# Optimization experiments

Measured on AMD Instinct MI355X. Metric: run time of the kernel, lower is better.

The kernel has to match this reference:

```python
import jax, jax.numpy as jnp
import numpy as np

C = 64  # channels fixed by module

def conv1x1(x, W, b):
    # x: [B,C,H,W], W: [C_out,C_in], b: [C_out]
    return jnp.einsum('bchw,oc->bohw', x, W) + b[None, :, None, None]

def setup_inputs() -> dict:
    key = jax.random.key(0)
    ks = jax.random.split(key, 16)
    B, H, W = 4, 64, 64
    inp = {
        'x_latter': jax.random.normal(ks[0], (B, C, H, W), jnp.float32),
        'x': jax.random.normal(ks[1], (B, C, H, W), jnp.float32),
    }
    scale = 1.0 / np.sqrt(C)
    names = ['high', 'low', 'value', 'e_conv', 'mid', 'latter']
    for i, n in enumerate(names):
        inp[f'W_{n}'] = jax.random.normal(ks[2 + 2 * i], (C, C), jnp.float32) * scale
        inp[f'b_{n}'] = jax.random.normal(ks[3 + 2 * i], (C,), jnp.float32) * 0.01
    return inp

def reference(x_latter, x, W_high, b_high, W_low, b_low, W_value, b_value,
              W_e_conv, b_e_conv, W_mid, b_mid, W_latter, b_latter):
    b, c, h, w = x_latter.shape
    hw = h * w
    # stage 1: channel-normalized spatial attention
    xl_hi = conv1x1(x_latter, W_high, b_high).reshape(b, c, hw)          # [b,c,hw]
    x_low = conv1x1(x, W_low, b_low).reshape(b, c, hw).transpose(0, 2, 1)  # [b,hw,c]
    p = jnp.einsum('bnc,bcm->bnm', x_low, xl_hi)                          # [b,hw,hw]
    p = jax.nn.softmax(p, axis=1)  # torch Softmax(dim=1) over first hw axis
    v = conv1x1(x, W_value, b_value).reshape(b, c, hw).transpose(0, 2, 1)  # [b,hw,c]
    e = jnp.einsum('bnm,bmc->bnc', p, v) + x_low                          # [b,hw,c]
    e = e.transpose(0, 2, 1).reshape(b, c, h, w)                          # [b,c,h,w]
    e = conv1x1(e, W_e_conv, b_e_conv).reshape(b, c, hw)                  # [b,c,hw]
    # stage 2: channel-channel attention
    xl2 = conv1x1(x_latter, W_latter, b_latter).reshape(b, c, hw).transpose(0, 2, 1)  # [b,hw,c]
    t = jnp.einsum('bcn,bnd->bcd', e, xl2)                                # [b,c,c]
    t = jax.nn.softmax(t, axis=1)
    x_mid = conv1x1(x, W_mid, b_mid).reshape(b, c, hw).transpose(0, 2, 1)  # [b,hw,c]
    out = jnp.einsum('bnc,bcd->bnd', x_mid, t)                            # [b,hw,c]
    return out.transpose(0, 2, 1).reshape(b, c, h, w)
```

## Files before the change

### kernel.cpp

```cpp
#include <hip/hip_runtime.h>
#include <math.h>

#define BATCH 4
#define CH 64
#define HW 4096
#define LOG2E 1.4426950408889634f

typedef __attribute__((ext_vector_type(8))) short short8;
typedef __attribute__((ext_vector_type(4))) float f32x4;
typedef __attribute__((ext_vector_type(4))) float float4v;
typedef __attribute__((ext_vector_type(4))) unsigned int uint4v;

#define MFMA(a, b, c) __builtin_amdgcn_mfma_f32_16x16x32_bf16(a, b, c, 0, 0, 0)

__device__ __forceinline__ float exp2v(float x) {
#if __has_builtin(__builtin_amdgcn_exp2f)
    return __builtin_amdgcn_exp2f(x);
#else
    return exp2f(x);
#endif
}
__device__ __forceinline__ void cvtpk2(float a, float b, unsigned &h, unsigned &l) {
    unsigned hv;
    asm("v_cvt_pk_bf16_f32 %0, %1, %2" : "=v"(hv) : "v"(a), "v"(b));
    float ra = a - __builtin_bit_cast(float, hv << 16);
    float rb = b - __builtin_bit_cast(float, hv & 0xffff0000u);
    unsigned lv;
    asm("v_cvt_pk_bf16_f32 %0, %1, %2" : "=v"(lv) : "v"(ra), "v"(rb));
    h = hv; l = lv;
}
__device__ __forceinline__ void gld16(const short* g, short* l) {
    __builtin_amdgcn_global_load_lds(
        (const __attribute__((address_space(1))) unsigned int*)g,
        (__attribute__((address_space(3))) unsigned int*)l, 16, 0, 0);
}

__global__ __launch_bounds__(256) void convm(
    const float* __restrict__ x, const float* __restrict__ xl,
    const float* __restrict__ Wlow, const float* __restrict__ blow,
    const float* __restrict__ Wval, const float* __restrict__ bval,
    const float* __restrict__ Wmid, const float* __restrict__ bmid,
    const float* __restrict__ Wlat, const float* __restrict__ blat,
    const float* __restrict__ Whigh, const float* __restrict__ bhigh,
    float* __restrict__ XLOW, float* __restrict__ XMID, float* __restrict__ XL2,
    short* __restrict__ PAh, short* __restrict__ PAl,
    short* __restrict__ PBh, short* __restrict__ PBl,
    short* __restrict__ PVh, short* __restrict__ PVl)
{
    int mode = blockIdx.z, b = blockIdx.y, bx = blockIdx.x;
    const float* W; const float* bias; const float* X;
    switch (mode) {
        case 0:  W = Wlow;  bias = blow;  X = x;  break;
        case 1:  W = Wval;  bias = bval;  X = x;  break;
        case 2:  W = Wmid;  bias = bmid;  X = x;  break;
        case 3:  W = Wlat;  bias = blat;  X = xl; break;
        default: W = Whigh; bias = bhigh; X = xl; break;
    }
    int t = threadIdx.x, wv = t >> 6, ln = t & 63;
    int row = ln & 15, g = ln >> 4;

    short8 Wh[4][2], Wlo[4][2];
    #pragma unroll
    for (int ot = 0; ot < 4; ot++)
        #pragma unroll
        for (int kt = 0; kt < 2; kt++) {
            const float* wp = W + (ot * 16 + row) * 64 + kt * 32 + g * 8;
            uint4v hw, lw;
            #pragma unroll
            for (int k2 = 0; k2 < 4; k2++) {
                unsigned h, l;
                cvtpk2(wp[2 * k2], wp[2 * k2 + 1], h, l);
                hw[k2] = h; lw[k2] = l;
            }
            Wh[ot][kt] = __builtin_bit_cast(short8, hw);
            Wlo[ot][kt] = __builtin_bit_cast(short8, lw);
        }

    int nt = bx * 4 + wv;
    short8 Bh[2], Bl[2];
    #pragma unroll
    for (int kt = 0; kt < 2; kt++) {
        float v[8];
        #pragma unroll
        for (int j = 0; j < 8; j++)
            v[j] = X[(size_t)(b * 64 + kt * 32 + g * 8 + j) * HW + nt * 16 + row];
        uint4v hw, lw;
        #pragma unroll
        for (int k2 = 0; k2 < 4; k2++) {
            unsigned h, l;
            cvtpk2(v[2 * k2], v[2 * k2 + 1], h, l);
            hw[k2] = h; lw[k2] = l;
        }
        Bh[kt] = __builtin_bit_cast(short8, hw);
        Bl[kt] = __builtin_bit_cast(short8, lw);
    }

    f32x4 acc[4];
    #pragma unroll
    for (int ot = 0; ot < 4; ot++) {
        #pragma unroll
        for (int r = 0; r < 4; r++) acc[ot][r] = bias[ot * 16 + g * 4 + r];
    }
    #pragma unroll
    for (int ot = 0; ot < 4; ot++)
        #pragma unroll
        for (int kt = 0; kt < 2; kt++) {
            acc[ot] = MFMA(Wh[ot][kt], Bh[kt], acc[ot]);
            acc[ot] = MFMA(Wh[ot][kt], Bl[kt], acc[ot]);
            acc[ot] = MFMA(Wlo[ot][kt], Bh[kt], acc[ot]);
        }

    __shared__ float Ld[64][65];
    #pragma unroll
    for (int ot = 0; ot < 4; ot++)
        #pragma unroll
        for (int r = 0; r < 4; r++)
            Ld[wv * 16 + (ln & 15)][ot * 16 + g * 4 + r] = acc[ot][r];
    __syncthreads();

    int n0 = bx * 64;
    if (mode == 0 || mode == 2 || mode == 3) {
        float* outp = (mode == 0) ? XLOW : (mode == 2) ? XMID : XL2;
        int n = t >> 2, o0 = (t & 3) * 16;
        float vout[16];
        #pragma unroll
        for (int k = 0; k < 16; k++) vout[k] = Ld[n][o0 + k];
        float* gp = outp + ((size_t)b * HW + n0 + n) * 64 + o0;
        #pragma unroll
        for (int k = 0; k < 4; k++)
            *(float4v*)(gp + k * 4) = *(float4v*)(vout + k * 4);
    }
    if (mode == 0 || mode == 4) {
        short* Ph = (mode == 0) ? PAh : PBh;
        short* Pl = (mode == 0) ? PAl : PBl;
        float scale = (mode == 4) ? LOG2E : 1.0f;
        #pragma unroll
        for (int kt = 0; kt < 2; kt++) {
            uint4v hw, lw;
            #pragma unroll
            for (int k2 = 0; k2 < 4; k2++) {
                unsigned h, l;
                cvtpk2(Ld[wv * 16 + (ln & 15)][kt * 32 + g * 8 + 2 * k2] * scale,
                       Ld[wv * 16 + (ln & 15)][kt * 32 + g * 8 + 2 * k2 + 1] * scale, h, l);
                hw[k2] = h; lw[k2] = l;
            }
            size_t blob = (((size_t)b * 256 + bx * 4 + wv) * 2 + kt) * 512 + (size_t)ln * 8;
            *(uint4v*)(Ph + blob) = hw;
            *(uint4v*)(Pl + blob) = lw;
        }
    }
    if (mode == 1) {
        int ktm_l = wv >> 1;
        int ct0 = (wv & 1) * 2;
        #pragma unroll
        for (int cc = 0; cc < 2; cc++) {
            int ct = ct0 + cc;
            int c = ct * 16 + (ln & 15);
            float v[8];
            #pragma unroll
            for (int j = 0; j < 8; j++)
                v[j] = Ld[(ktm_l * 2 + (j >> 2)) * 16 + g * 4 + (j & 3)][c];
            uint4v hw, lw;
            #pragma unroll
            for (int k2 = 0; k2 < 4; k2++) {
                unsigned h, l;
                cvtpk2(v[2 * k2], v[2 * k2 + 1], h, l);
                hw[k2] = h; lw[k2] = l;
            }
            size_t blob = (((size_t)b * 128 + bx * 2 + ktm_l) * 4 + ct) * 512 + (size_t)ln * 8;
            *(uint4v*)(PVh + blob) = hw;
            *(uint4v*)(PVl + blob) = lw;
        }
    }
}

__global__ __launch_bounds__(256) void zpass2(
    const short* __restrict__ PAh, const short* __restrict__ PAl,
    const short* __restrict__ PBh, const short* __restrict__ PBl,
    float* __restrict__ Zp)
{
    int bid = blockIdx.x;
    int sw = (bid & 7) * 128 + (bid >> 3);
    int mchunk = sw & 63, nc = (sw >> 6) & 3, b = sw >> 8;
    int t = threadIdx.x, wv = t >> 6, ln = t & 63;
    short8 bh[4][2], bl[4][2];
    #pragma unroll
    for (int msub = 0; msub < 4; msub++)
        #pragma unroll
        for (int kt = 0; kt < 2; kt++) {
            size_t o = ((size_t)(b * 256 + mchunk * 4 + msub) * 2 + kt) * 512 + ln * 8;
            bh[msub][kt] = *(const short8*)(PBh + o);
            bl[msub][kt] = *(const short8*)(PBl + o);
        }
    float zacc[4] = {0.f, 0.f, 0.f, 0.f};
    for (int s = 0; s < 16; s++) {
        int nt = nc * 64 + s * 4 + wv;
        size_t ab = ((size_t)(b * 256 + nt) * 2) * 512 + ln * 8;
        short8 ah0 = *(const short8*)(PAh + ab);
        short8 ah1 = *(const short8*)(PAh + ab + 512);
        short8 al0 = *(const short8*)(PAl + ab);
        short8 al1 = *(const short8*)(PAl + ab + 512);
        #pragma unroll
        for (int msub = 0; msub < 4; msub++) {
            f32x4 acc = {0.f, 0.f, 0.f, 0.f};
            acc = MFMA(ah0, bh[msub][0], acc);
            acc = MFMA(ah1, bh[msub][1], acc);
            acc = MFMA(ah0, bl[msub][0], acc);
            acc = MFMA(ah1, bl[msub][1], acc);
            acc = MFMA(al0, bh[msub][0], acc);
            acc = MFMA(al1, bh[msub][1], acc);
            zacc[msub] += exp2v(acc[0]) + exp2v(acc[1]) + exp2v(acc[2]) + exp2v(acc[3]);
        }
    }
    #pragma unroll
    for (int msub = 0; msub < 4; msub++) {
        zacc[msub] += __shfl_xor(zacc[msub], 16, 64);
        zacc[msub] += __shfl_xor(zacc[msub], 32, 64);
    }
    __shared__ float sZ[4][64];
    if (ln < 16) {
        #pragma unroll
        for (int msub = 0; msub < 4; msub++) sZ[wv][msub * 16 + ln] = zacc[msub];
    }
    __syncthreads();
    if (t < 64) {
        float z = sZ[0][t] + sZ[1][t] + sZ[2][t] + sZ[3][t];
        Zp[((size_t)(b * 4 + nc)) * 4096 + mchunk * 64 + t] = z;
    }
}

__global__ __launch_bounds__(256, 3) void epass10(
    const short* __restrict__ PAh, const short* __restrict__ PAl,
    const short* __restrict__ PBh, const short* __restrict__ PBl,
    const short* __restrict__ PVh, const short* __restrict__ PVl,
    const float* __restrict__ Zp, float* __restrict__ Ep, int nseg)
{
    int nwg = 32 * nseg * 4, cpx = nwg >> 3;
    int bid = blockIdx.x;
    int sw = (bid & 7) * cpx + (bid >> 3);
    int nb = sw & 31, mseg = (sw >> 5) % nseg, b = sw / (32 * nseg);
    int iters = 128 / nseg;
    int mper = 4096 / nseg;
    int t = threadIdx.x, wv = t >> 6, ln = t & 63;
    int lnm = ln & 15, lnr = ln >> 4;

    __shared__ __align__(16) short sB[2][2][2048];
    __shared__ __align__(16) short sV[2][2][2048];
    __shared__ __align__(16) float sZi[1024];

    for (int k = t; k < mper; k += 256) {
        int m = mseg * mper + k;
        float z = Zp[((size_t)(b * 4 + 0)) * 4096 + m]
                + Zp[((size_t)(b * 4 + 1)) * 4096 + m]
                + Zp[((size_t)(b * 4 + 2)) * 4096 + m]
                + Zp[((size_t)(b * 4 + 3)) * 4096 + m];
        sZi[k] = 1.f / z;
    }

    short8 Lh[2][2], Ll[2][2];
    #pragma unroll
    for (int rt = 0; rt < 2; rt++)
        #pragma unroll
        for (int kt = 0; kt < 2; kt++) {
            int nt = nb * 8 + wv * 2 + rt;
            size_t base = ((size_t)(b * 256 + nt) * 2 + kt) * 512 + ln * 8;
            Lh[rt][kt] = *(const short8*)(PAh + base);
            Ll[rt][kt] = *(const short8*)(PAl + base);
        }

    f32x4 acc_e[2][4];
    #pragma unroll
    for (int rt = 0; rt < 2; rt++)
        #pragma unroll
        for (int ct = 0; ct < 4; ct++) acc_e[rt][ct] = (f32x4){0.f, 0.f, 0.f, 0.f};

    const int mt00 = mseg * (mper >> 4);
    const int ktm0 = mseg * (mper >> 5);
    #define STAGE(bufi, ii) { \
        size_t pbb = (size_t)b * 262144 + (size_t)(mt00 + (ii) * 2) * 1024; \
        size_t pvb = (size_t)b * 262144 + (size_t)(ktm0 + (ii)) * 2048; \
        gld16(PBh + pbb + t * 8, &sB[bufi][0][wv * 512]); \
        gld16(PBl + pbb + t * 8, &sB[bufi][1][wv * 512]); \
        gld16(PVh + pvb + t * 8, &sV[bufi][0][wv * 512]); \
        gld16(PVl + pvb + t * 8, &sV[bufi][1][wv * 512]); }

    STAGE(0, 0);
    __syncthreads();

    for (int i = 0; i < iters; i++) {
        int cur = i & 1;
        if (i + 1 < iters) STAGE(cur ^ 1, i + 1);

        f32x4 wf[2][2];
        #pragma unroll
        for (int ms = 0; ms < 2; ms++) {
            const short8 bh0 = *(const short8*)&sB[cur][0][(ms * 2 + 0) * 512 + ln * 8];
            const short8 bh1 = *(const short8*)&sB[cur][0][(ms * 2 + 1) * 512 + ln * 8];
            const short8 bl0 = *(const short8*)&sB[cur][1][(ms * 2 + 0) * 512 + ln * 8];
            const short8 bl1 = *(const short8*)&sB[cur][1][(ms * 2 + 1) * 512 + ln * 8];
            const f32x4 vz = *(const f32x4*)&sZi[i * 32 + ms * 16 + lnr * 4];
            __builtin_amdgcn_s_setprio(1);
            #pragma unroll
            for (int rt = 0; rt < 2; rt++) {
                f32x4 acc = {0.f, 0.f, 0.f, 0.f};
                acc = MFMA(bh0, Lh[rt][0], acc);
                acc = MFMA(bh1, Lh[rt][1], acc);
                acc = MFMA(bh0, Ll[rt][0], acc);
                acc = MFMA(bh1, Ll[rt][1], acc);
                acc = MFMA(bl0, Lh[rt][0], acc);
                acc = MFMA(bl1, Lh[rt][1], acc);
                #pragma unroll
                for (int r = 0; r < 4; r++)
                    wf[rt][ms][r] = exp2v(acc[r]) * vz[r];
            }
            __builtin_amdgcn_s_setprio(0);
        }
        short8 pah[2], pal[2];
        #pragma unroll
        for (int rt = 0; rt < 2; rt++) {
            uint4v hw, lw;
            #pragma unroll
            for (int k2 = 0; k2 < 4; k2++) {
                unsigned h, l;
                cvtpk2(wf[rt][k2 >> 1][2 * (k2 & 1)],
                       wf[rt][k2 >> 1][2 * (k2 & 1) + 1], h, l);
                hw[k2] = h; lw[k2] = l;
            }
            pah[rt] = __builtin_bit_cast(short8, hw);
            pal[rt] = __builtin_bit_cast(short8, lw);
        }
        __builtin_amdgcn_s_setprio(1);
        #pragma unroll
        for (int ct = 0; ct < 4; ct++) {
            const short8 vh = *(const short8*)&sV[cur][0][ct * 512 + ln * 8];
            const short8 vl = *(const short8*)&sV[cur][1][ct * 512 + ln * 8];
            #pragma unroll
            for (int rt = 0; rt < 2; rt++) {
                acc_e[rt][ct] = MFMA(pah[rt], vh, acc_e[rt][ct]);
                acc_e[rt][ct] = MFMA(pah[rt], vl, acc_e[rt][ct]);
                acc_e[rt][ct] = MFMA(pal[rt], vh, acc_e[rt][ct]);
            }
        }
        __builtin_amdgcn_s_setprio(0);
        __syncthreads();
    }
    #undef STAGE

    float* ep = Ep + ((size_t)mseg * BATCH + b) * HW * 64;
    #pragma unroll
    for (int rt = 0; rt < 2; rt++) {
        int n0 = (nb * 8 + wv * 2 + rt) * 16 + lnr * 4;
        #pragma unroll
        for (int ct = 0; ct < 4; ct++) {
            #pragma unroll
            for (int r = 0; r < 4; r++)
                ep[(size_t)(n0 + r) * 64 + ct * 16 + lnm] = acc_e[rt][ct][r];
        }
    }
}

template <int NSEG>
__global__ __launch_bounds__(256) void econv6(
    const float* __restrict__ Ep, const float* __restrict__ XLOW,
    const float* __restrict__ W, const float* __restrict__ bias,
    float* __restrict__ E2)
{
    const size_t SEG = (size_t)BATCH * HW * 64;
    int b = blockIdx.y, n0 = blockIdx.x * 64, t = threadIdx.x;
    __shared__ float Wl[64][64];
    __shared__ float El[64][65];
    for (int i = t; i < 4096; i += 256) Wl[i >> 6][i & 63] = W[i];
    for (int q = t; q < 1024; q += 256) {
        int nl = q >> 4, c0 = (q & 15) * 4;
        size_t idx = ((size_t)b * HW + n0 + nl) * 64 + c0;
        float4v s = *(const float4v*)(XLOW + idx);
        #pragma unroll
        for (int sg = 0; sg < NSEG; sg++) {
            float4v p = *(const float4v*)(Ep + sg * SEG + idx);
            s.x += p.x; s.y += p.y; s.z += p.z; s.w += p.w;
        }
        El[nl][c0] = s.x; El[nl][c0 + 1] = s.y;
        El[nl][c0 + 2] = s.z; El[nl][c0 + 3] = s.w;
    }
    __syncthreads();
    int nl = t & 63, og = t >> 6;
    for (int k = 0; k < 16; k++) {
        int o = og * 16 + k;
        float a0 = bias[o], a1 = 0.f, a2 = 0.f, a3 = 0.f;
        #pragma unroll
        for (int c = 0; c < 64; c += 4) {
            a0 += Wl[o][c]     * El[nl][c];
            a1 += Wl[o][c + 1] * El[nl][c + 1];
            a2 += Wl[o][c + 2] * El[nl][c + 2];
            a3 += Wl[o][c + 3] * El[nl][c + 3];
        }
        E2[((size_t)b * 64 + o) * HW + n0 + nl] = (a0 + a1) + (a2 + a3);
    }
}

__global__ __launch_bounds__(1024) void tmat(
    const float* __restrict__ E2, const float* __restrict__ XL2, float* __restrict__ T)
{
    int b = blockIdx.y, c = blockIdx.x, t = threadIdx.x;
    int d = t & 63, nl = t >> 6;
    const float* e = E2 + ((size_t)b * 64 + c) * HW;
    const float* x2 = XL2 + (size_t)b * HW * 64;
    float a0 = 0.f, a1 = 0.f;
    #pragma unroll 4
    for (int k = 0; k < 256; k += 2) {
        int na = k * 16 + nl, nb2 = na + 16;
        a0 += e[na] * x2[(size_t)na * 64 + d];
        a1 += e[nb2] * x2[(size_t)nb2 * 64 + d];
    }
    __shared__ float red[16][64];
    red[nl][d] = a0 + a1;
    __syncthreads();
    if (t < 64) {
        float s = 0.f;
        #pragma unroll
        for (int j = 0; j < 16; j++) s += red[j][t];
        T[((size_t)b * 64 + c) * 64 + t] = s;
    }
}

__global__ __launch_bounds__(64) void softT(
    const float* __restrict__ T, float* __restrict__ Ts)
{
    int d = blockIdx.x, b = blockIdx.y, c = threadIdx.x;
    float v = T[((size_t)b * 64 + c) * 64 + d];
    float M = v;
    #pragma unroll
    for (int o = 32; o > 0; o >>= 1) M = fmaxf(M, __shfl_xor(M, o, 64));
    float ez = __expf(v - M);
    float Z = ez;
    #pragma unroll
    for (int o = 32; o > 0; o >>= 1) Z += __shfl_xor(Z, o, 64);
    Ts[((size_t)b * 64 + c) * 64 + d] = ez / Z;
}

__global__ __launch_bounds__(256) void outk(
    const float* __restrict__ XMID, const float* __restrict__ Ts, float* __restrict__ out)
{
    int b = blockIdx.y, n0 = blockIdx.x * 64, t = threadIdx.x;
    __shared__ float Xm[64][65];
    __shared__ float Tl[64][64];
    for (int i = t; i < 4096; i += 256) {
        int nl = i >> 6, c = i & 63;
        Xm[nl][c] = XMID[((size_t)b * HW + n0 + nl) * 64 + c];
    }
    for (int i = t; i < 4096; i += 256) Tl[i >> 6][i & 63] = Ts[(size_t)b * 4096 + i];
    __syncthreads();
    int nl = t & 63, dg = t >> 6;
    float accs[16];
    #pragma unroll
    for (int k = 0; k < 16; k++) accs[k] = 0.f;
    for (int c = 0; c < 64; c++) {
        float xv = Xm[nl][c];
        #pragma unroll
        for (int k = 0; k < 16; k++) accs[k] += xv * Tl[c][dg * 16 + k];
    }
    #pragma unroll
    for (int k = 0; k < 16; k++) {
        int d = dg * 16 + k;
        out[((size_t)b * 64 + d) * HW + n0 + nl] = accs[k];
    }
}

extern "C" void kernel_launch(void* const* d_in, const int* in_sizes, int n_in,
                              void* d_out, int out_size, void* d_ws, size_t ws_size,
                              hipStream_t stream)
{
    const float* x_latter = (const float*)d_in[0];
    const float* x        = (const float*)d_in[1];
    const float* W_high = (const float*)d_in[2];  const float* b_high = (const float*)d_in[3];
    const float* W_low  = (const float*)d_in[4];  const float* b_low  = (const float*)d_in[5];
    const float* W_val  = (const float*)d_in[6];  const float* b_val  = (const float*)d_in[7];
    const float* W_ec   = (const float*)d_in[8];  const float* b_ec   = (const float*)d_in[9];
    const float* W_mid  = (const float*)d_in[10]; const float* b_mid  = (const float*)d_in[11];
    const float* W_lat  = (const float*)d_in[12]; const float* b_lat  = (const float*)d_in[13];
    float* outp = (float*)d_out;

    const size_t MAT = (size_t)BATCH * CH * HW;

    const size_t fixed_f = 3 * MAT + (size_t)BATCH * 4 * HW + 2 * (size_t)BATCH * 64 * 64;
    const size_t need8 = (fixed_f + 8 * MAT) * 4 + 6 * MAT * 2;
    int nseg = (ws_size >= need8) ? 8 : 4;

    float* ws = (float*)d_ws;
    size_t off = 0;
    float* XLOW = ws + off; off += MAT;
    float* XMID = ws + off; off += MAT;
    float* XL2  = ws + off; off += MAT;
    float* Zp   = ws + off; off += (size_t)BATCH * 4 * HW;
    float* T    = ws + off; off += (size_t)BATCH * 64 * 64;
    float* Ts   = ws + off; off += (size_t)BATCH * 64 * 64;
    short* sp = (short*)(ws + off);
    short* PAh = sp; sp += MAT;
    short* PAl = sp; sp += MAT;
    short* PBh = sp; sp += MAT;
    short* PBl = sp; sp += MAT;
    short* PVh = sp; sp += MAT;
    short* PVl = sp; sp += MAT;
    float* Ep  = (float*)sp;
    float* E2  = (float*)PAh;

    convm<<<dim3(64, BATCH, 5), 256, 0, stream>>>(
        x, x_latter, W_low, b_low, W_val, b_val, W_mid, b_mid, W_lat, b_lat,
        W_high, b_high, XLOW, XMID, XL2, PAh, PAl, PBh, PBl, PVh, PVl);
    zpass2<<<dim3(1024), 256, 0, stream>>>(PAh, PAl, PBh, PBl, Zp);
    epass10<<<dim3(32 * nseg * 4), 256, 0, stream>>>(
        PAh, PAl, PBh, PBl, PVh, PVl, Zp, Ep, nseg);
    if (nseg == 8)
        econv6<8><<<dim3(64, BATCH), 256, 0, stream>>>(Ep, XLOW, W_ec, b_ec, E2);
    else
        econv6<4><<<dim3(64, BATCH), 256, 0, stream>>>(Ep, XLOW, W_ec, b_ec, E2);
    tmat<<<dim3(64, BATCH), 1024, 0, stream>>>(E2, XL2, T);
    softT<<<dim3(64, BATCH), 64, 0, stream>>>(T, Ts);
    outk<<<dim3(64, BATCH), 256, 0, stream>>>(XMID, Ts, outp);
}
```

Baseline: 139.5 us.

## Prepack conv weights once and split T matmul into LDS-tiled partials

Measured after the change: 147.9 us. 1.06x slower.

```diff
diff --git a/kernel.cpp b/kernel.cpp
--- a/kernel.cpp
+++ b/kernel.cpp
@@ -35,26 +35,56 @@
         (__attribute__((address_space(3))) unsigned int*)l, 16, 0, 0);
 }
 
+__global__ __launch_bounds__(256) void wpack(
+    const float* __restrict__ Wlow, const float* __restrict__ Wval,
+    const float* __restrict__ Wmid, const float* __restrict__ Wlat,
+    const float* __restrict__ Whigh,
+    short* __restrict__ WFh, short* __restrict__ WFl)
+{
+    int mode = blockIdx.x;
+    const float* W;
+    switch (mode) {
+        case 0: W = Wlow; break;  case 1: W = Wval; break;
+        case 2: W = Wmid; break;  case 3: W = Wlat; break;
+        default: W = Whigh; break;
+    }
+    int t = threadIdx.x, ot = t >> 6, ln = t & 63;
+    int row = ln & 15, g = ln >> 4;
+    #pragma unroll
+    for (int kt = 0; kt < 2; kt++) {
+        const float* wp = W + (ot * 16 + row) * 64 + kt * 32 + g * 8;
+        uint4v hw, lw;
+        #pragma unroll
+        for (int k2 = 0; k2 < 4; k2++) {
+            unsigned h, l;
+            cvtpk2(wp[2 * k2], wp[2 * k2 + 1], h, l);
+            hw[k2] = h; lw[k2] = l;
+        }
+        size_t blob = ((size_t)(mode * 8 + ot * 2 + kt)) * 512 + (size_t)ln * 8;
+        *(uint4v*)(WFh + blob) = hw;
+        *(uint4v*)(WFl + blob) = lw;
+    }
+}
+
 __global__ __launch_bounds__(256) void convm(
     const float* __restrict__ x, const float* __restrict__ xl,
-    const float* __restrict__ Wlow, const float* __restrict__ blow,
-    const float* __restrict__ Wval, const float* __restrict__ bval,
-    const float* __restrict__ Wmid, const float* __restrict__ bmid,
-    const float* __restrict__ Wlat, const float* __restrict__ blat,
-    const float* __restrict__ Whigh, const float* __restrict__ bhigh,
+    const short* __restrict__ WFh, const short* __restrict__ WFl,
+    const float* __restrict__ blow, const float* __restrict__ bval,
+    const float* __restrict__ bmid, const float* __restrict__ blat,
+    const float* __restrict__ bhigh,
     float* __restrict__ XLOW, float* __restrict__ XMID, float* __restrict__ XL2,
     short* __restrict__ PAh, short* __restrict__ PAl,
     short* __restrict__ PBh, short* __restrict__ PBl,
     short* __restrict__ PVh, short* __restrict__ PVl)
 {
     int mode = blockIdx.z, b = blockIdx.y, bx = blockIdx.x;
-    const float* W; const float* bias; const float* X;
+    const float* bias; const float* X;
     switch (mode) {
-        case 0:  W = Wlow;  bias = blow;  X = x;  break;
-        case 1:  W = Wval;  bias = bval;  X = x;  break;
-        case 2:  W = Wmid;  bias = bmid;  X = x;  break;
-        case 3:  W = Wlat;  bias = blat;  X = xl; break;
-        default: W = Whigh; bias = bhigh; X = xl; break;
+        case 0:  bias = blow;  X = x;  break;
+        case 1:  bias = bval;  X = x;  break;
+        case 2:  bias = bmid;  X = x;  break;
+        case 3:  bias = blat;  X = xl; break;
+        default: bias = bhigh; X = xl; break;
     }
     int t = threadIdx.x, wv = t >> 6, ln = t & 63;
     int row = ln & 15, g = ln >> 4;
@@ -64,16 +94,9 @@
     for (int ot = 0; ot < 4; ot++)
         #pragma unroll
         for (int kt = 0; kt < 2; kt++) {
-            const float* wp = W + (ot * 16 + row) * 64 + kt * 32 + g * 8;
-            uint4v hw, lw;
-            #pragma unroll
-            for (int k2 = 0; k2 < 4; k2++) {
-                unsigned h, l;
-                cvtpk2(wp[2 * k2], wp[2 * k2 + 1], h, l);
-                hw[k2] = h; lw[k2] = l;
-            }
-            Wh[ot][kt] = __builtin_bit_cast(short8, hw);
-            Wlo[ot][kt] = __builtin_bit_cast(short8, lw);
+            size_t blob = ((size_t)(mode * 8 + ot * 2 + kt)) * 512 + (size_t)ln * 8;
+            Wh[ot][kt] = *(const short8*)(WFh + blob);
+            Wlo[ot][kt] = *(const short8*)(WFl + blob);
         }
 
     int nt = bx * 4 + wv;
@@ -398,44 +421,71 @@
     }
 }
 
-__global__ __launch_bounds__(1024) void tmat(
-    const float* __restrict__ E2, const float* __restrict__ XL2, float* __restrict__ T)
-{
-    int b = blockIdx.y, c = blockIdx.x, t = threadIdx.x;
-    int d = t & 63, nl = t >> 6;
-    const float* e = E2 + ((size_t)b * 64 + c) * HW;
-    const float* x2 = XL2 + (size_t)b * HW * 64;
-    float a0 = 0.f, a1 = 0.f;
-    #pragma unroll 4
-    for (int k = 0; k < 256; k += 2) {
-        int na = k * 16 + nl, nb2 = na + 16;
-        a0 += e[na] * x2[(size_t)na * 64 + d];
-        a1 += e[nb2] * x2[(size_t)nb2 * 64 + d];
-    }
-    __shared__ float red[16][64];
-    red[nl][d] = a0 + a1;
+__global__ __launch_bounds__(256) void tmat2(
+    const float* __restrict__ E2, const float* __restrict__ XL2, float* __restrict__ Tp)
+{
+    int b = blockIdx.y, ch = blockIdx.x;
+    int t = threadIdx.x;
+    __shared__ float Xs[128][64];
+    int n0 = ch * 128;
+    for (int i = t; i < 8192; i += 256) {
+        int nl = i >> 6, d = i & 63;
+        Xs[nl][d] = XL2[((size_t)b * HW + n0 + nl) * 64 + d];
+    }
+    __syncthreads();
+    int c = t & 63, dg = t >> 6;
+    const float* e2row = E2 + ((size_t)b * 64 + c) * HW + n0;
+    float acc[16];
+    #pragma unroll
+    for (int k = 0; k < 16; k++) acc[k] = 0.f;
+    for (int q = 0; q < 32; q++) {
+        float4v ev = *(const float4v*)(e2row + q * 4);
+        #pragma unroll
+        for (int r = 0; r < 4; r++) {
+            float e = (r == 0) ? ev.x : (r == 1) ? ev.y : (r == 2) ? ev.z : ev.w;
+            int nl = q * 4 + r;
+            const float4v xa = *(const float4v*)&Xs[nl][dg * 16];
+            const float4v xb = *(const float4v*)&Xs[nl][dg * 16 + 4];
+            const float4v xc = *(const float4v*)&Xs[nl][dg * 16 + 8];
+            const float4v xd = *(const float4v*)&Xs[nl][dg * 16 + 12];
+            acc[0] += e * xa.x; acc[1] += e * xa.y; acc[2] += e * xa.z; acc[3] += e * xa.w;
+            acc[4] += e * xb.x; acc[5] += e * xb.y; acc[6] += e * xb.z; acc[7] += e * xb.w;
+            acc[8] += e * xc.x; acc[9] += e * xc.y; acc[10] += e * xc.z; acc[11] += e * xc.w;
+            acc[12] += e * xd.x; acc[13] += e * xd.y; acc[14] += e * xd.z; acc[15] += e * xd.w;
+        }
+    }
+    float* tp = Tp + ((size_t)(ch * BATCH + b)) * 4096 + c * 64 + dg * 16;
+    #pragma unroll
+    for (int k = 0; k < 4; k++)
+        *(float4v*)(tp + k * 4) = *(float4v*)(acc + k * 4);
+}
+
+__global__ __launch_bounds__(256) void softTsum(
+    const float* __restrict__ Tp, float* __restrict__ Ts)
+{
+    int b = blockIdx.x, t = threadIdx.x;
+    __shared__ float Tl[64][65];
+    __shared__ float Md[64], Zd[64];
+    for (int i = t; i < 4096; i += 256) {
+        float s = 0.f;
+        #pragma unroll 8
+        for (int ch = 0; ch < 32; ch++)
+            s += Tp[((size_t)(ch * BATCH + b)) * 4096 + i];
+        Tl[i >> 6][i & 63] = s;
+    }
     __syncthreads();
     if (t < 64) {
-        float s = 0.f;
-        #pragma unroll
-        for (int j = 0; j < 16; j++) s += red[j][t];
-        T[((size_t)b * 64 + c) * 64 + t] = s;
-    }
-}
-
-__global__ __launch_bounds__(64) void softT(
-    const float* __restrict__ T, float* __restrict__ Ts)
-{
-    int d = blockIdx.x, b = blockIdx.y, c = threadIdx.x;
-    float v = T[((size_t)b * 64 + c) * 64 + d];
-    float M = v;
-    #pragma unroll
-    for (int o = 32; o > 0; o >>= 1) M = fmaxf(M, __shfl_xor(M, o, 64));
-    float ez = __expf(v - M);
-    float Z = ez;
-    #pragma unroll
-    for (int o = 32; o > 0; o >>= 1) Z += __shfl_xor(Z, o, 64);
-    Ts[((size_t)b * 64 + c) * 64 + d] = ez / Z;
+        float M = Tl[0][t];
+        for (int c = 1; c < 64; c++) M = fmaxf(M, Tl[c][t]);
+        float Z = 0.f;
+        for (int c = 0; c < 64; c++) Z += __expf(Tl[c][t] - M);
+        Md[t] = M; Zd[t] = 1.f / Z;
+    }
+    __syncthreads();
+    for (int i = t; i < 4096; i += 256) {
+        int c = i >> 6, d = i & 63;
+        Ts[(size_t)b * 4096 + i] = __expf(Tl[c][d] - Md[d]) * Zd[d];
+    }
 }
 
 __global__ __launch_bounds__(256) void outk(
@@ -481,9 +531,11 @@
     float* outp = (float*)d_out;
 
     const size_t MAT = (size_t)BATCH * CH * HW;
-
-    const size_t fixed_f = 3 * MAT + (size_t)BATCH * 4 * HW + 2 * (size_t)BATCH * 64 * 64;
-    const size_t need8 = (fixed_f + 8 * MAT) * 4 + 6 * MAT * 2;
+    const size_t TPN = (size_t)32 * BATCH * 4096;
+    const size_t WFN = (size_t)5 * 8 * 512;
+
+    const size_t fixed_f = 3 * MAT + (size_t)BATCH * 4 * HW + TPN + (size_t)BATCH * 4096;
+    const size_t need8 = (fixed_f + 8 * MAT) * 4 + (6 * MAT + 2 * WFN) * 2;
     int nseg = (ws_size >= need8) ? 8 : 4;
 
     float* ws = (float*)d_ws;
@@ -492,8 +544,8 @@
     float* XMID = ws + off; off += MAT;
     float* XL2  = ws + off; off += MAT;
     float* Zp   = ws + off; off += (size_t)BATCH * 4 * HW;
-    float* T    = ws + off; off += (size_t)BATCH * 64 * 64;
-    float* Ts   = ws + off; off += (size_t)BATCH * 64 * 64;
+    float* Tp   = ws + off; off += TPN;
+    float* Ts   = ws + off; off += (size_t)BATCH * 4096;
     short* sp = (short*)(ws + off);
     short* PAh = sp; sp += MAT;
     short* PAl = sp; sp += MAT;
@@ -501,12 +553,15 @@
     short* PBl = sp; sp += MAT;
     short* PVh = sp; sp += MAT;
     short* PVl = sp; sp += MAT;
+    short* WFh = sp; sp += WFN;
+    short* WFl = sp; sp += WFN;
     float* Ep  = (float*)sp;
     float* E2  = (float*)PAh;
 
+    wpack<<<dim3(5), 256, 0, stream>>>(W_low, W_val, W_mid, W_lat, W_high, WFh, WFl);
     convm<<<dim3(64, BATCH, 5), 256, 0, stream>>>(
-        x, x_latter, W_low, b_low, W_val, b_val, W_mid, b_mid, W_lat, b_lat,
-        W_high, b_high, XLOW, XMID, XL2, PAh, PAl, PBh, PBl, PVh, PVl);
+        x, x_latter, WFh, WFl, b_low, b_val, b_mid, b_lat, b_high,
+        XLOW, XMID, XL2, PAh, PAl, PBh, PBl, PVh, PVl);
     zpass2<<<dim3(1024), 256, 0, stream>>>(PAh, PAl, PBh, PBl, Zp);
     epass10<<<dim3(32 * nseg * 4), 256, 0, stream>>>(
         PAh, PAl, PBh, PBl, PVh, PVl, Zp, Ep, nseg);
@@ -514,7 +569,7 @@
         econv6<8><<<dim3(64, BATCH), 256, 0, stream>>>(Ep, XLOW, W_ec, b_ec, E2);
     else
         econv6<4><<<dim3(64, BATCH), 256, 0, stream>>>(Ep, XLOW, W_ec, b_ec, E2);
-    tmat<<<dim3(64, BATCH), 1024, 0, stream>>>(E2, XL2, T);
-    softT<<<dim3(64, BATCH), 64, 0, stream>>>(T, Ts);
+    tmat2<<<dim3(32, BATCH), 256, 0, stream>>>(E2, XL2, Tp);
+    softTsum<<<dim3(BATCH), 256, 0, stream>>>(Tp, Ts);
     outk<<<dim3(64, BATCH), 256, 0, stream>>>(XMID, Ts, outp);
 }
```

## Split epass work across eight waves, one row tile per wave

Applied to the files above, without the earlier changes.

After: 225.5 us. 61.7% more time.

```diff
diff --git a/kernel.cpp b/kernel.cpp
--- a/kernel.cpp
+++ b/kernel.cpp
@@ -229,7 +229,7 @@
     }
 }
 
-__global__ __launch_bounds__(256, 3) void epass10(
+__global__ __launch_bounds__(512, 8) void epass11(
     const short* __restrict__ PAh, const short* __restrict__ PAl,
     const short* __restrict__ PBh, const short* __restrict__ PBl,
     const short* __restrict__ PVh, const short* __restrict__ PVl,
@@ -248,7 +248,7 @@
     __shared__ __align__(16) short sV[2][2][2048];
     __shared__ __align__(16) float sZi[1024];
 
-    for (int k = t; k < mper; k += 256) {
+    for (int k = t; k < mper; k += 512) {
         int m = mseg * mper + k;
         float z = Zp[((size_t)(b * 4 + 0)) * 4096 + m]
                 + Zp[((size_t)(b * 4 + 1)) * 4096 + m]
@@ -257,32 +257,31 @@
         sZi[k] = 1.f / z;
     }
 
-    short8 Lh[2][2], Ll[2][2];
-    #pragma unroll
-    for (int rt = 0; rt < 2; rt++)
-        #pragma unroll
-        for (int kt = 0; kt < 2; kt++) {
-            int nt = nb * 8 + wv * 2 + rt;
-            size_t base = ((size_t)(b * 256 + nt) * 2 + kt) * 512 + ln * 8;
-            Lh[rt][kt] = *(const short8*)(PAh + base);
-            Ll[rt][kt] = *(const short8*)(PAl + base);
-        }
-
-    f32x4 acc_e[2][4];
-    #pragma unroll
-    for (int rt = 0; rt < 2; rt++)
-        #pragma unroll
-        for (int ct = 0; ct < 4; ct++) acc_e[rt][ct] = (f32x4){0.f, 0.f, 0.f, 0.f};
+    int nt = nb * 8 + wv;
+    short8 Lh[2], Ll[2];
+    #pragma unroll
+    for (int kt = 0; kt < 2; kt++) {
+        size_t base = ((size_t)(b * 256 + nt) * 2 + kt) * 512 + ln * 8;
+        Lh[kt] = *(const short8*)(PAh + base);
+        Ll[kt] = *(const short8*)(PAl + base);
+    }
+
+    f32x4 acc_e[4];
+    #pragma unroll
+    for (int ct = 0; ct < 4; ct++) acc_e[ct] = (f32x4){0.f, 0.f, 0.f, 0.f};
 
     const int mt00 = mseg * (mper >> 4);
     const int ktm0 = mseg * (mper >> 5);
+    const int arr_ = wv >> 1, half_ = wv & 1;
     #define STAGE(bufi, ii) { \
         size_t pbb = (size_t)b * 262144 + (size_t)(mt00 + (ii) * 2) * 1024; \
         size_t pvb = (size_t)b * 262144 + (size_t)(ktm0 + (ii)) * 2048; \
-        gld16(PBh + pbb + t * 8, &sB[bufi][0][wv * 512]); \
-        gld16(PBl + pbb + t * 8, &sB[bufi][1][wv * 512]); \
-        gld16(PVh + pvb + t * 8, &sV[bufi][0][wv * 512]); \
-        gld16(PVl + pvb + t * 8, &sV[bufi][1][wv * 512]); }
+        const short* gsrc = (arr_ == 0) ? PBh + pbb : (arr_ == 1) ? PBl + pbb \
+                          : (arr_ == 2) ? PVh + pvb : PVl + pvb; \
+        short* ldst = (arr_ == 0) ? &sB[bufi][0][0] : (arr_ == 1) ? &sB[bufi][1][0] \
+                    : (arr_ == 2) ? &sV[bufi][0][0] : &sV[bufi][1][0]; \
+        gld16(gsrc + half_ * 1024 + ln * 8,       ldst + half_ * 1024); \
+        gld16(gsrc + half_ * 1024 + 512 + ln * 8, ldst + half_ * 1024 + 512); }
 
     STAGE(0, 0);
     __syncthreads();
@@ -291,7 +290,7 @@
         int cur = i & 1;
         if (i + 1 < iters) STAGE(cur ^ 1, i + 1);
 
-        f32x4 wf[2][2];
+        f32x4 wf[2];
         #pragma unroll
         for (int ms = 0; ms < 2; ms++) {
             const short8 bh0 = *(const short8*)&sB[cur][0][(ms * 2 + 0) * 512 + ln * 8];
@@ -300,46 +299,39 @@
             const short8 bl1 = *(const short8*)&sB[cur][1][(ms * 2 + 1) * 512 + ln * 8];
             const f32x4 vz = *(const f32x4*)&sZi[i * 32 + ms * 16 + lnr * 4];
             __builtin_amdgcn_s_setprio(1);
+            f32x4 acc = {0.f, 0.f, 0.f, 0.f};
+            acc = MFMA(bh0, Lh[0], acc);
+            acc = MFMA(bh1, Lh[1], acc);
+            acc = MFMA(bh0, Ll[0], acc);
+            acc = MFMA(bh1, Ll[1], acc);
+            acc = MFMA(bl0, Lh[0], acc);
+            acc = MFMA(bl1, Lh[1], acc);
+            __builtin_amdgcn_s_setprio(0);
             #pragma unroll
-            for (int rt = 0; rt < 2; rt++) {
-                f32x4 acc = {0.f, 0.f, 0.f, 0.f};
-                acc = MFMA(bh0, Lh[rt][0], acc);
-                acc = MFMA(bh1, Lh[rt][1], acc);
-                acc = MFMA(bh0, Ll[rt][0], acc);
-                acc = MFMA(bh1, Ll[rt][1], acc);
-                acc = MFMA(bl0, Lh[rt][0], acc);
-                acc = MFMA(bl1, Lh[rt][1], acc);
-                #pragma unroll
-                for (int r = 0; r < 4; r++)
-                    wf[rt][ms][r] = exp2v(acc[r]) * vz[r];
-            }
-            __builtin_amdgcn_s_setprio(0);
-        }
-        short8 pah[2], pal[2];
-        #pragma unroll
-        for (int rt = 0; rt < 2; rt++) {
+            for (int r = 0; r < 4; r++)
+                wf[ms][r] = exp2v(acc[r]) * vz[r];
+        }
+        short8 pah, pal;
+        {
             uint4v hw, lw;
             #pragma unroll
             for (int k2 = 0; k2 < 4; k2++) {
                 unsigned h, l;
-                cvtpk2(wf[rt][k2 >> 1][2 * (k2 & 1)],
-                       wf[rt][k2 >> 1][2 * (k2 & 1) + 1], h, l);
+                cvtpk2(wf[k2 >> 1][2 * (k2 & 1)],
+                       wf[k2 >> 1][2 * (k2 & 1) + 1], h, l);
                 hw[k2] = h; lw[k2] = l;
             }
-            pah[rt] = __builtin_bit_cast(short8, hw);
-            pal[rt] = __builtin_bit_cast(short8, lw);
+            pah = __builtin_bit_cast(short8, hw);
+            pal = __builtin_bit_cast(short8, lw);
         }
         __builtin_amdgcn_s_setprio(1);
         #pragma unroll
         for (int ct = 0; ct < 4; ct++) {
             const short8 vh = *(const short8*)&sV[cur][0][ct * 512 + ln * 8];
             const short8 vl = *(const short8*)&sV[cur][1][ct * 512 + ln * 8];
-            #pragma unroll
-            for (int rt = 0; rt < 2; rt++) {
-                acc_e[rt][ct] = MFMA(pah[rt], vh, acc_e[rt][ct]);
-                acc_e[rt][ct] = MFMA(pah[rt], vl, acc_e[rt][ct]);
-                acc_e[rt][ct] = MFMA(pal[rt], vh, acc_e[rt][ct]);
-            }
+            acc_e[ct] = MFMA(pah, vh, acc_e[ct]);
+            acc_e[ct] = MFMA(pah, vl, acc_e[ct]);
+            acc_e[ct] = MFMA(pal, vh, acc_e[ct]);
         }
         __builtin_amdgcn_s_setprio(0);
         __syncthreads();
@@ -347,15 +339,12 @@
     #undef STAGE
 
     float* ep = Ep + ((size_t)mseg * BATCH + b) * HW * 64;
-    #pragma unroll
-    for (int rt = 0; rt < 2; rt++) {
-        int n0 = (nb * 8 + wv * 2 + rt) * 16 + lnr * 4;
-        #pragma unroll
-        for (int ct = 0; ct < 4; ct++) {
-            #pragma unroll
-            for (int r = 0; r < 4; r++)
-                ep[(size_t)(n0 + r) * 64 + ct * 16 + lnm] = acc_e[rt][ct][r];
-        }
+    int n0 = nt * 16 + lnr * 4;
+    #pragma unroll
+    for (int ct = 0; ct < 4; ct++) {
+        #pragma unroll
+        for (int r = 0; r < 4; r++)
+            ep[(size_t)(n0 + r) * 64 + ct * 16 + lnm] = acc_e[ct][r];
     }
 }
 
@@ -508,7 +497,7 @@
         x, x_latter, W_low, b_low, W_val, b_val, W_mid, b_mid, W_lat, b_lat,
         W_high, b_high, XLOW, XMID, XL2, PAh, PAl, PBh, PBl, PVh, PVl);
     zpass2<<<dim3(1024), 256, 0, stream>>>(PAh, PAl, PBh, PBl, Zp);
-    epass10<<<dim3(32 * nseg * 4), 256, 0, stream>>>(
+    epass11<<<dim3(32 * nseg * 4), 512, 0, stream>>>(
         PAh, PAl, PBh, PBl, PVh, PVl, Zp, Ep, nseg);
     if (nseg == 8)
         econv6<8><<<dim3(64, BATCH), 256, 0, stream>>>(Ep, XLOW, W_ec, b_ec, E2);
```
